# Kernel optimization log

Hardware: AMD Instinct MI355X
Metric: run time of the kernel (lower is better)

The kernel has to match this reference:

```python
import jax, jax.numpy as jnp
import numpy as np

D_MODEL = 1024
N_HEADS = 16
D_HEAD = D_MODEL // N_HEADS


def setup_inputs() -> dict:
    key = jax.random.key(0)
    ks = jax.random.split(key, 5)
    s_in = 1.0 / np.sqrt(D_MODEL)
    x = jax.random.normal(ks[0], (4, 2048, D_MODEL), dtype=jnp.float32)
    W_qkv = jax.random.uniform(ks[1], (D_MODEL, 3 * D_MODEL), jnp.float32, -s_in, s_in)
    b_qkv = jax.random.uniform(ks[2], (3 * D_MODEL,), jnp.float32, -s_in, s_in)
    W_out = jax.random.uniform(ks[3], (D_MODEL, D_MODEL), jnp.float32, -s_in, s_in)
    b_out = jax.random.uniform(ks[4], (D_MODEL,), jnp.float32, -s_in, s_in)
    return {"x": x, "W_qkv": W_qkv, "b_qkv": b_qkv, "W_out": W_out, "b_out": b_out}


def reference(x, W_qkv, b_qkv, W_out, b_out):
    B, T, C = x.shape
    qkv = x @ W_qkv + b_qkv                       # [B,T,3C]
    q, k, v = jnp.split(qkv, 3, axis=-1)
    # [B,T,C] -> [B,H,T,Dh]
    def heads(t):
        return t.reshape(B, T, N_HEADS, D_HEAD).transpose(0, 2, 1, 3)
    q, k, v = heads(q), heads(k), heads(v)
    scale = 1.0 / np.sqrt(D_HEAD).astype(np.float32)
    attn = jnp.einsum('bhqd,bhkd->bhqk', q, k) * scale   # [B,H,T,T]
    causal = jnp.tril(jnp.ones((T, T), dtype=bool))
    attn = jnp.where(causal, attn, -jnp.inf)
    attn_weights = jax.nn.softmax(attn, axis=-1)
    out = jnp.einsum('bhqk,bhkd->bhqd', attn_weights, v)  # [B,H,T,Dh]
    out = out.transpose(0, 2, 1, 3).reshape(B, T, C)
    return out @ W_out + b_out
```

## Files before the change

### kernel.cpp

```cpp
#include <hip/hip_runtime.h>
#include <hip/hip_bf16.h>

#define BATCH   4
#define SEQ     2048
#define DMODEL  1024
#define NHEADS  16
#define DHEAD   64
#define MROWS   (BATCH*SEQ)
#define QKV_N   (3*DMODEL)
#define NEG_BIG (-1.0e30f)
#define WS_NEED ((size_t)MROWS * 2*DMODEL * sizeof(__hip_bfloat16))
#define SCALE_Q 0.18033688011112042f

using bf16 = __hip_bfloat16;
typedef __attribute__((ext_vector_type(8))) short short8;
typedef __attribute__((ext_vector_type(4))) float floatx4;

__device__ __align__(16) unsigned short g_wqT[QKV_N * DMODEL];
__device__ __align__(16) unsigned short g_woT[DMODEL * DMODEL];
__device__ __align__(16) unsigned short g_xb [MROWS * DMODEL];

__device__ __forceinline__ unsigned short f2bf_rne(float f) {
    union { bf16 b; unsigned short u; } t;
    t.b = __float2bfloat16(f);
    return t.u;
}

__device__ __forceinline__ void gload_lds16(const void* g, void* l) {
    __builtin_amdgcn_global_load_lds(
        (const __attribute__((address_space(1))) unsigned*)g,
        (__attribute__((address_space(3))) unsigned*)l, 16, 0, 0);
}

__global__ __launch_bounds__(256) void cast_x(const float* __restrict__ x) {
    const size_t i = ((size_t)blockIdx.x*256 + threadIdx.x)*8;
    const float4 a = *(const float4*)(x + i);
    const float4 b = *(const float4*)(x + i + 4);
    union { uint4 u4; unsigned short us[8]; } o;
    o.us[0]=f2bf_rne(a.x); o.us[1]=f2bf_rne(a.y); o.us[2]=f2bf_rne(a.z); o.us[3]=f2bf_rne(a.w);
    o.us[4]=f2bf_rne(b.x); o.us[5]=f2bf_rne(b.y); o.us[6]=f2bf_rne(b.z); o.us[7]=f2bf_rne(b.w);
    *(uint4*)(g_xb + i) = o.u4;
}

__global__ __launch_bounds__(256) void transcast_w2(
    const float* __restrict__ Wq, const float* __restrict__ Wo)
{
    const int bx = blockIdx.x;
    const float* W;
    unsigned short* dst;
    int N, n0;
    if (bx < 48) { W = Wq; dst = g_wqT; N = QKV_N;  n0 = bx * 64; }
    else         { W = Wo; dst = g_woT; N = DMODEL; n0 = (bx - 48) * 64; }
    const int k0 = blockIdx.y * 64;

    __shared__ unsigned short T[64][72];
    const int tid = threadIdx.x;
    const int r = tid >> 2, c0 = (tid & 3) * 16;

#pragma unroll
    for (int it = 0; it < 4; ++it) {
        const float4 v = *(const float4*)(W + (size_t)(k0 + r)*N + n0 + c0 + it*4);
        T[r][c0 + it*4 + 0] = f2bf_rne(v.x);
        T[r][c0 + it*4 + 1] = f2bf_rne(v.y);
        T[r][c0 + it*4 + 2] = f2bf_rne(v.z);
        T[r][c0 + it*4 + 3] = f2bf_rne(v.w);
    }
    __syncthreads();
    const int nr = tid >> 2, kc0 = (tid & 3) * 16;
#pragma unroll
    for (int it = 0; it < 2; ++it) {
        union { uint4 u4; unsigned short us[8]; } o;
#pragma unroll
        for (int j = 0; j < 8; j++) o.us[j] = T[kc0 + it*8 + j][nr];
        *(uint4*)(dst + (size_t)(n0 + nr)*DMODEL + k0 + kc0 + it*8) = o.u4;
    }
}

__global__ __launch_bounds__(512, 2) void qkv_proj(
    const float* __restrict__ bias, bf16* __restrict__ Qo,
    bf16* __restrict__ Ko, bf16* __restrict__ VT)
{
    const unsigned short* A  = g_xb;
    const unsigned short* BT = g_wqT;
    constexpr int NBN = 12;
    constexpr int NWG = 32 * NBN;

    __shared__ __align__(16) char smem[131072];
    char* const sA = smem;
    char* const sB = smem + 65536;

    const int orig = blockIdx.x;
    const int wgid = (orig & 7) * (NWG >> 3) + (orig >> 3);
    const int bm = wgid / NBN, bn = wgid % NBN;

    const int tid  = threadIdx.x;
    const int w    = tid >> 6, lane = tid & 63;
    const int m16  = lane & 15, quad = lane >> 4;
    const int rw   = w >> 2, cw = w & 3;

    const int rL = lane >> 2;
    const int cD = (lane & 3) ^ ((lane >> 3) & 3);
    const unsigned short* gA = A  + (size_t)(bm*256 + rL)*DMODEL + cD*8;
    const unsigned short* gB = BT + (size_t)(bn*256 + rL)*DMODEL + cD*8;

    const int laneRd = m16*64 + (quad ^ ((m16 >> 1) & 3))*16;

    floatx4 acc[8][4];
#pragma unroll
    for (int i = 0; i < 8; ++i)
#pragma unroll
        for (int j = 0; j < 4; ++j) {
            acc[i][j][0]=0.f; acc[i][j][1]=0.f; acc[i][j][2]=0.f; acc[i][j][3]=0.f;
        }

    auto stA = [&](int buf, int rg, int kh, int k0) {
        gload_lds16(gA + (size_t)(rg*16)*DMODEL + k0 + kh*32,
                    sA + buf*32768 + (rg*2 + kh)*1024);
    };
    auto stB = [&](int buf, int rg, int kh, int k0) {
        gload_lds16(gB + (size_t)(rg*16)*DMODEL + k0 + kh*32,
                    sB + buf*32768 + (rg*2 + kh)*1024);
    };

    stA(0, w, 0, 0);   stA(0, 8+w, 0, 0);
    stB(0, 2*w, 0, 0); stB(0, 2*w+1, 0, 0);
    stA(0, w, 1, 0);   stA(0, 8+w, 1, 0);
    stB(0, 2*w, 1, 0); stB(0, 2*w+1, 1, 0);
    asm volatile("s_waitcnt vmcnt(0)" ::: "memory");
    __builtin_amdgcn_s_barrier();

    const int NT = DMODEL / 64;
    for (int t = 0; t < NT; ++t) {
        const int  buf = t & 1;
        const int  k1  = (t + 1) * 64;
        const bool st  = (t + 1 < NT);
        char* const Ab = sA + buf*32768;
        char* const Bb = sB + buf*32768;

        short8 bf[4], af[4];

#pragma unroll
        for (int j = 0; j < 4; ++j)
            bf[j] = *(const short8*)(Bb + ((cw*4 + j)*2 + 0)*1024 + laneRd);
#pragma unroll
        for (int i = 0; i < 4; ++i)
            af[i] = *(const short8*)(Ab + ((rw*8 + i)*2 + 0)*1024 + laneRd);
        if (st) { stA(buf^1, w, 0, k1); stA(buf^1, 8+w, 0, k1); }
        __builtin_amdgcn_s_barrier();
        __builtin_amdgcn_s_setprio(1);
#pragma unroll
        for (int i = 0; i < 4; ++i)
#pragma unroll
            for (int j = 0; j < 4; ++j)
                acc[i][j] = __builtin_amdgcn_mfma_f32_16x16x32_bf16(af[i], bf[j], acc[i][j], 0, 0, 0);
        __builtin_amdgcn_s_setprio(0);
        __builtin_amdgcn_s_barrier();

#pragma unroll
        for (int i = 0; i < 4; ++i)
            af[i] = *(const short8*)(Ab + ((rw*8 + 4 + i)*2 + 0)*1024 + laneRd);
        if (st) { stB(buf^1, 2*w, 0, k1); stB(buf^1, 2*w+1, 0, k1); }
        __builtin_amdgcn_s_barrier();
        __builtin_amdgcn_s_setprio(1);
#pragma unroll
        for (int i = 0; i < 4; ++i)
#pragma unroll
            for (int j = 0; j < 4; ++j)
                acc[4+i][j] = __builtin_amdgcn_mfma_f32_16x16x32_bf16(af[i], bf[j], acc[4+i][j], 0, 0, 0);
        __builtin_amdgcn_s_setprio(0);
        if (st) { asm volatile("s_waitcnt vmcnt(4)" ::: "memory"); }
        else    { asm volatile("s_waitcnt vmcnt(0)" ::: "memory"); }
        __builtin_amdgcn_s_barrier();

#pragma unroll
        for (int j = 0; j < 4; ++j)
            bf[j] = *(const short8*)(Bb + ((cw*4 + j)*2 + 1)*1024 + laneRd);
#pragma unroll
        for (int i = 0; i < 4; ++i)
            af[i] = *(const short8*)(Ab + ((rw*8 + i)*2 + 1)*1024 + laneRd);
        if (st) { stA(buf^1, w, 1, k1); stA(buf^1, 8+w, 1, k1); }
        __builtin_amdgcn_s_barrier();
        __builtin_amdgcn_s_setprio(1);
#pragma unroll
        for (int i = 0; i < 4; ++i)
#pragma unroll
            for (int j = 0; j < 4; ++j)
                acc[i][j] = __builtin_amdgcn_mfma_f32_16x16x32_bf16(af[i], bf[j], acc[i][j], 0, 0, 0);
        __builtin_amdgcn_s_setprio(0);
        __builtin_amdgcn_s_barrier();

#pragma unroll
        for (int i = 0; i < 4; ++i)
            af[i] = *(const short8*)(Ab + ((rw*8 + 4 + i)*2 + 1)*1024 + laneRd);
        if (st) { stB(buf^1, 2*w, 1, k1); stB(buf^1, 2*w+1, 1, k1); }
        __builtin_amdgcn_s_barrier();
        __builtin_amdgcn_s_setprio(1);
#pragma unroll
        for (int i = 0; i < 4; ++i)
#pragma unroll
            for (int j = 0; j < 4; ++j)
                acc[4+i][j] = __builtin_amdgcn_mfma_f32_16x16x32_bf16(af[i], bf[j], acc[4+i][j], 0, 0, 0);
        __builtin_amdgcn_s_setprio(0);
        if (st) {
            asm volatile("s_waitcnt vmcnt(4)" ::: "memory");
            __builtin_amdgcn_s_barrier();
        }
    }

    float bv[4];
#pragma unroll
    for (int j = 0; j < 4; ++j)
        bv[j] = bias[bn*256 + cw*64 + j*16 + m16];

    const int seg = bn >> 2;
    if (seg < 2) {
        bf16* Cout = seg ? Ko : Qo;
        const float sc = seg ? 1.0f : SCALE_Q;
#pragma unroll
        for (int mf = 0; mf < 8; ++mf)
#pragma unroll
            for (int r = 0; r < 4; ++r) {
                const int gm = bm*256 + rw*128 + mf*16 + quad*4 + r;
#pragma unroll
                for (int j = 0; j < 4; ++j) {
                    const int cc = (bn*256 + cw*64 + j*16 + m16) & 1023;
                    Cout[(size_t)gm*DMODEL + cc] =
                        __float2bfloat16((acc[mf][j][r] + bv[j]) * sc);
                }
            }
    } else {
#pragma unroll
        for (int mf = 0; mf < 8; ++mf) {
            const int gm0 = bm*256 + rw*128 + mf*16 + quad*4;
            const int bb = gm0 >> 11, t0 = gm0 & 2047;
#pragma unroll
            for (int j = 0; j < 4; ++j) {
                const int cv = ((bn & 3)*256 + cw*64 + j*16 + m16);
                const int hh = cv >> 6, dd = cv & 63;
                union { unsigned long long u8; unsigned short us[4]; } o;
#pragma unroll
                for (int r = 0; r < 4; ++r)
                    o.us[r] = f2bf_rne(acc[mf][j][r] + bv[j]);
                *(unsigned long long*)(VT
                    + ((size_t)((bb*NHEADS + hh)*DHEAD + dd))*SEQ + t0) = o.u8;
            }
        }
    }
}

__global__ __launch_bounds__(512, 2) void out_proj(
    const void* __restrict__ Av, const float* __restrict__ bias, float* C)
{
    const unsigned short* A  = (const unsigned short*)Av;
    const unsigned short* BT = g_woT;
    constexpr int NBN = 8;
    constexpr int NWG = NBN * 32;

    __shared__ __align__(16) char smem[98304];
    char* const sA = smem;
    char* const sB = smem + 65536;

    const int orig = blockIdx.x;
    const int wgid = (orig & 7) * (NWG >> 3) + (orig >> 3);
    const int bm = wgid / NBN, bn = wgid % NBN;

    const int tid  = threadIdx.x;
    const int w    = tid >> 6, lane = tid & 63;
    const int m16  = lane & 15, quad = lane >> 4;
    const int rw   = w >> 1, cw = w & 1;

    const int rL = lane >> 2;
    const int cD = (lane & 3) ^ ((lane >> 3) & 3);
    const unsigned short* gA = A  + (size_t)(bm*256 + rL)*DMODEL + cD*8;
    const unsigned short* gB = BT + (size_t)(bn*128 + rL)*DMODEL + cD*8;

    const int laneRd = m16*64 + (quad ^ ((m16 >> 1) & 3))*16;

    floatx4 acc[2][2][4];
#pragma unroll
    for (int q = 0; q < 2; ++q)
#pragma unroll
        for (int i = 0; i < 2; ++i)
#pragma unroll
            for (int j = 0; j < 4; ++j) {
                acc[q][i][j][0]=0.f; acc[q][i][j][1]=0.f;
                acc[q][i][j][2]=0.f; acc[q][i][j][3]=0.f;
            }

    auto stageA = [&](int buf, int a, int k0) {
        const int rg = 4*a + (w >> 1), kh = w & 1;
        gload_lds16(gA + (size_t)(rg*16)*DMODEL + k0 + kh*32,
                    sA + buf*32768 + (rg*2 + kh)*1024);
    };
    auto stageB = [&](int buf, int b, int k0) {
        const int rg = 4*b + (w >> 1), kh = w & 1;
        gload_lds16(gB + (size_t)(rg*16)*DMODEL + k0 + kh*32,
                    sB + buf*16384 + (rg*2 + kh)*1024);
    };

    stageB(0, 0, 0); stageB(0, 1, 0);
    stageA(0, 0, 0); stageA(0, 1, 0); stageA(0, 2, 0); stageA(0, 3, 0);
    asm volatile("s_waitcnt vmcnt(0)" ::: "memory");
    __builtin_amdgcn_s_barrier();

    const int NT = DMODEL / 64;
    for (int t = 0; t < NT; ++t) {
        const int  buf = t & 1;
        const int  k1  = (t + 1) * 64;
        const bool st  = (t + 1 < NT);
        char* const Ab = sA + buf*32768;
        char* const Bb = sB + buf*16384;

        short8 bf[4][2], af[2][2];
#pragma unroll
        for (int j = 0; j < 4; ++j)
#pragma unroll
            for (int kh = 0; kh < 2; ++kh)
                bf[j][kh] = *(const short8*)(Bb + ((cw*4 + j)*2 + kh)*1024 + laneRd);
#pragma unroll
        for (int i = 0; i < 2; ++i)
#pragma unroll
            for (int kh = 0; kh < 2; ++kh)
                af[i][kh] = *(const short8*)(Ab + ((rw*2 + i)*2 + kh)*1024 + laneRd);

        if (st) { stageB(buf^1, 0, k1); stageB(buf^1, 1, k1);
                  stageA(buf^1, 0, k1); stageA(buf^1, 1, k1); }
        __builtin_amdgcn_s_barrier();

        __builtin_amdgcn_s_setprio(1);
#pragma unroll
        for (int i = 0; i < 2; ++i)
#pragma unroll
            for (int j = 0; j < 4; ++j) {
                acc[0][i][j] = __builtin_amdgcn_mfma_f32_16x16x32_bf16(
                    af[i][0], bf[j][0], acc[0][i][j], 0, 0, 0);
                acc[0][i][j] = __builtin_amdgcn_mfma_f32_16x16x32_bf16(
                    af[i][1], bf[j][1], acc[0][i][j], 0, 0, 0);
            }
        __builtin_amdgcn_s_setprio(0);

        if (st) { asm volatile("s_waitcnt vmcnt(4)" ::: "memory"); }
        else    { asm volatile("s_waitcnt vmcnt(0)" ::: "memory"); }
        __builtin_amdgcn_s_barrier();

#pragma unroll
        for (int i = 0; i < 2; ++i)
#pragma unroll
            for (int kh = 0; kh < 2; ++kh)
                af[i][kh] = *(const short8*)(Ab + ((8 + rw*2 + i)*2 + kh)*1024 + laneRd);

        if (st) { stageA(buf^1, 2, k1); stageA(buf^1, 3, k1); }
        __builtin_amdgcn_s_barrier();

        __builtin_amdgcn_s_setprio(1);
#pragma unroll
        for (int i = 0; i < 2; ++i)
#pragma unroll
            for (int j = 0; j < 4; ++j) {
                acc[1][i][j] = __builtin_amdgcn_mfma_f32_16x16x32_bf16(
                    af[i][0], bf[j][0], acc[1][i][j], 0, 0, 0);
                acc[1][i][j] = __builtin_amdgcn_mfma_f32_16x16x32_bf16(
                    af[i][1], bf[j][1], acc[1][i][j], 0, 0, 0);
            }
        __builtin_amdgcn_s_setprio(0);

        if (st) { asm volatile("s_waitcnt vmcnt(2)" ::: "memory"); }
        else    { asm volatile("s_waitcnt vmcnt(0)" ::: "memory"); }
        __builtin_amdgcn_s_barrier();
    }

    float bv[4];
#pragma unroll
    for (int j = 0; j < 4; ++j)
        bv[j] = bias[bn*128 + cw*64 + j*16 + m16];

#pragma unroll
    for (int q = 0; q < 2; ++q)
#pragma unroll
        for (int i = 0; i < 2; ++i)
#pragma unroll
            for (int r = 0; r < 4; ++r) {
                const int gm = bm*256 + q*128 + rw*32 + i*16 + quad*4 + r;
#pragma unroll
                for (int j = 0; j < 4; ++j) {
                    const int cc = bn*128 + cw*64 + j*16 + m16;
                    C[(size_t)gm*DMODEL + cc] = acc[q][i][j][r] + bv[j];
                }
            }
}

__global__ __launch_bounds__(256, 3) void attn_mfma7(
    const bf16* __restrict__ Qg, const bf16* __restrict__ Kg,
    const bf16* __restrict__ VTg, bf16* __restrict__ Og)
{
    __shared__ alignas(16) unsigned short Kt[2][64][72];
    __shared__ alignas(16) unsigned short Vt[80][72];
    __shared__ alignas(16) unsigned short Ps[4][32][72];

    const int L  = blockIdx.x;
    const int qt = 15 - (L >> 6);
    const int bh = L & 63;
    const int b  = bh >> 4, h = bh & 15;

    const int tid = threadIdx.x;
    const int w = tid >> 6, lane = tid & 63;
    const int m16 = lane & 15, quad = lane >> 4;
    const int sr = tid >> 2, sc0 = (tid & 3) * 8;
    const size_t bhs = (size_t)(b*NHEADS + h);

    const int nkt = 2*qt + 2;
    const int qrow0 = qt*128 + w*32;

    short8 qf[2][2];
#pragma unroll
    for (int i = 0; i < 2; ++i)
#pragma unroll
        for (int c = 0; c < 2; ++c)
            qf[i][c] = *(const short8*)(Qg + (size_t)(b*SEQ + qrow0 + i*16 + m16)*DMODEL
                                        + h*DHEAD + c*32 + quad*8);

    floatx4 of[2][5];
    float mrow[2];
#pragma unroll
    for (int i = 0; i < 2; ++i) {
        mrow[i] = NEG_BIG;
#pragma unroll
        for (int nt = 0; nt < 5; ++nt) { of[i][nt][0]=0.f; of[i][nt][1]=0.f; of[i][nt][2]=0.f; of[i][nt][3]=0.f; }
    }

    for (int idx = tid; idx < 16*72; idx += 256) {
        const int r = idx / 72, c = idx % 72;
        Vt[64 + r][c] = (r == 0) ? (unsigned short)0x3F80 : (unsigned short)0;
    }

    {
        const bf16* kp = Kg  + (size_t)(b*SEQ + sr)*DMODEL + h*DHEAD + sc0;
        const bf16* vp = VTg + (bhs*DHEAD + sr)*SEQ + sc0;
        const uint4 a0 = *(const uint4*)kp, a1 = *(const uint4*)(kp + 32);
        const uint4 b0 = *(const uint4*)vp, b1 = *(const uint4*)(vp + 32);
        *(uint4*)&Kt[0][sr][sc0]      = a0;
        *(uint4*)&Kt[0][sr][sc0 + 32] = a1;
        *(uint4*)&Vt[sr][sc0]         = b0;
        *(uint4*)&Vt[sr][sc0 + 32]    = b1;
        __syncthreads();
    }

    for (int kt = 0; kt < nkt; ++kt) {
        const int buf = kt & 1;
        const int k064 = kt * 64;
        const bool pre = (kt + 1 < nkt);
        uint4 kr0, kr1, vr0, vr1;
        if (pre) {
            const bf16* kp = Kg  + (size_t)(b*SEQ + k064 + 64 + sr)*DMODEL + h*DHEAD + sc0;
            const bf16* vp = VTg + (bhs*DHEAD + sr)*SEQ + k064 + 64 + sc0;
            kr0 = *(const uint4*)kp; kr1 = *(const uint4*)(kp + 32);
            vr0 = *(const uint4*)vp; vr1 = *(const uint4*)(vp + 32);
        }

        floatx4 sf[2][4];
#pragma unroll
        for (int t4 = 0; t4 < 4; ++t4) {
            const short8 kf0 = *(const short8*)&Kt[buf][t4*16 + m16][quad*8];
            const short8 kf1 = *(const short8*)&Kt[buf][t4*16 + m16][32 + quad*8];
#pragma unroll
            for (int i = 0; i < 2; ++i) {
                floatx4 a; a[0]=0.f; a[1]=0.f; a[2]=0.f; a[3]=0.f;
                a = __builtin_amdgcn_mfma_f32_16x16x32_bf16(kf0, qf[i][0], a, 0, 0, 0);
                a = __builtin_amdgcn_mfma_f32_16x16x32_bf16(kf1, qf[i][1], a, 0, 0, 0);
                sf[i][t4] = a;
            }
        }

        const bool need_mask = (k064 + 63 > qrow0);
#pragma unroll
        for (int i = 0; i < 2; ++i) {
            if (need_mask) {
                const int qg = qrow0 + i*16 + m16;
#pragma unroll
                for (int t4 = 0; t4 < 4; ++t4)
#pragma unroll
                    for (int r = 0; r < 4; ++r)
                        if (k064 + t4*16 + quad*4 + r > qg) sf[i][t4][r] = NEG_BIG;
            }
            float mx = sf[i][0][0];
#pragma unroll
            for (int t4 = 0; t4 < 4; ++t4)
#pragma unroll
                for (int r = 0; r < 4; ++r) mx = fmaxf(mx, sf[i][t4][r]);
            mx = fmaxf(mx, __shfl_xor(mx, 16));
            mx = fmaxf(mx, __shfl_xor(mx, 32));

            if (__any(mx > mrow[i] + 8.f)) {
                const float mnew  = fmaxf(mrow[i], mx);
                const float alpha = exp2f(mrow[i] - mnew);
                mrow[i] = mnew;
#pragma unroll
                for (int nt = 0; nt < 5; ++nt)
#pragma unroll
                    for (int r = 0; r < 4; ++r) of[i][nt][r] *= alpha;
            }

#pragma unroll
            for (int t4 = 0; t4 < 4; ++t4)
#pragma unroll
                for (int r = 0; r < 4; ++r)
                    sf[i][t4][r] = exp2f(sf[i][t4][r] - mrow[i]);

#pragma unroll
            for (int t4 = 0; t4 < 4; ++t4) {
                union { unsigned long long u8; unsigned short us[4]; } o;
#pragma unroll
                for (int r = 0; r < 4; ++r) o.us[r] = f2bf_rne(sf[i][t4][r]);
                *(unsigned long long*)&Ps[w][i*16 + m16][t4*16 + quad*4] = o.u8;
            }
        }

        short8 pf[2][2];
#pragma unroll
        for (int i = 0; i < 2; ++i)
#pragma unroll
            for (int c = 0; c < 2; ++c)
                pf[i][c] = *(const short8*)&Ps[w][i*16 + m16][c*32 + quad*8];
#pragma unroll
        for (int nt = 0; nt < 5; ++nt) {
            const short8 vf0 = *(const short8*)&Vt[nt*16 + m16][quad*8];
            const short8 vf1 = *(const short8*)&Vt[nt*16 + m16][32 + quad*8];
#pragma unroll
            for (int i = 0; i < 2; ++i) {
                of[i][nt] = __builtin_amdgcn_mfma_f32_16x16x32_bf16(vf0, pf[i][0], of[i][nt], 0, 0, 0);
                of[i][nt] = __builtin_amdgcn_mfma_f32_16x16x32_bf16(vf1, pf[i][1], of[i][nt], 0, 0, 0);
            }
        }

        __syncthreads();
        if (pre) {
            *(uint4*)&Kt[buf^1][sr][sc0]      = kr0;
            *(uint4*)&Kt[buf^1][sr][sc0 + 32] = kr1;
            *(uint4*)&Vt[sr][sc0]             = vr0;
            *(uint4*)&Vt[sr][sc0 + 32]        = vr1;
        }
        __syncthreads();
    }

#pragma unroll
    for (int i = 0; i < 2; ++i) {
        const float lsum = __shfl(of[i][4][0], m16);
        const float rl = 1.f / fmaxf(lsum, 1e-20f);
        const size_t rowbase = (size_t)(b*SEQ + qrow0 + i*16 + m16)*DMODEL + h*DHEAD;
#pragma unroll
        for (int nt = 0; nt < 4; ++nt) {
            union { unsigned long long u8; unsigned short us[4]; } o;
#pragma unroll
            for (int r = 0; r < 4; ++r) o.us[r] = f2bf_rne(of[i][nt][r] * rl);
            *(unsigned long long*)(Og + rowbase + nt*16 + quad*4) = o.u8;
        }
    }
}

__global__ void diag_fill(float* out, int n, float val) {
    int i = blockIdx.x*blockDim.x + threadIdx.x;
    if (i < n) out[i] = val;
}

extern "C" void kernel_launch(void* const* d_in, const int* in_sizes, int n_in,
                              void* d_out, int out_size, void* d_ws, size_t ws_size,
                              hipStream_t stream) {
    const float* x     = (const float*)d_in[0];
    const float* W_qkv = (const float*)d_in[1];
    const float* b_qkv = (const float*)d_in[2];
    const float* W_out = (const float*)d_in[3];
    const float* b_out = (const float*)d_in[4];

    if (ws_size < WS_NEED) {
        const float val = 100.f + (float)(ws_size >> 20);
        diag_fill<<<(out_size + 255)/256, 256, 0, stream>>>((float*)d_out, out_size, val);
        return;
    }

    bf16* Qb  = (bf16*)d_out;
    bf16* VTb = (bf16*)d_out + (size_t)MROWS*DMODEL;
    bf16* Kb  = (bf16*)d_ws;
    bf16* Ob  = (bf16*)d_ws + (size_t)MROWS*DMODEL;

    cast_x<<<MROWS*DMODEL/2048, 256, 0, stream>>>(x);
    {
        dim3 g(64, DMODEL/64);
        transcast_w2<<<g, 256, 0, stream>>>(W_qkv, W_out);
    }
    qkv_proj<<<384, 512, 0, stream>>>(b_qkv, Qb, Kb, VTb);
    attn_mfma7<<<1024, 256, 0, stream>>>(Qb, Kb, VTb, Ob);
    out_proj<<<256, 512, 0, stream>>>(Ob, b_out, (float*)d_out);
}
```

Before: 266.9 us.

## Merge prep kernels and simplify GEMM main loops to one barrier per k-step

Fuses the x cast and weight transpose-cast into a single prep launch, removing one kernel launch. In both the QKV and output projection GEMMs, the k-step is restructured: all of the next tile is staged at once, and all A/B fragments for each k-half are loaded before one big MFMA batch. This replaces several intra-iteration barriers and partial vmcnt waits with a single full wait and barrier. It reduces sync overhead but holds more fragment registers and gives the prefetch less overlap before the full wait.

```diff
diff --git a/kernel.cpp b/kernel.cpp
--- a/kernel.cpp
+++ b/kernel.cpp
@@ -32,31 +32,32 @@
         (__attribute__((address_space(3))) unsigned*)l, 16, 0, 0);
 }
 
-__global__ __launch_bounds__(256) void cast_x(const float* __restrict__ x) {
-    const size_t i = ((size_t)blockIdx.x*256 + threadIdx.x)*8;
-    const float4 a = *(const float4*)(x + i);
-    const float4 b = *(const float4*)(x + i + 4);
-    union { uint4 u4; unsigned short us[8]; } o;
-    o.us[0]=f2bf_rne(a.x); o.us[1]=f2bf_rne(a.y); o.us[2]=f2bf_rne(a.z); o.us[3]=f2bf_rne(a.w);
-    o.us[4]=f2bf_rne(b.x); o.us[5]=f2bf_rne(b.y); o.us[6]=f2bf_rne(b.z); o.us[7]=f2bf_rne(b.w);
-    *(uint4*)(g_xb + i) = o.u4;
-}
-
-__global__ __launch_bounds__(256) void transcast_w2(
-    const float* __restrict__ Wq, const float* __restrict__ Wo)
+__global__ __launch_bounds__(256) void prep(
+    const float* __restrict__ x, const float* __restrict__ Wq,
+    const float* __restrict__ Wo)
 {
     const int bx = blockIdx.x;
+    const int tid = threadIdx.x;
+    if (bx < 4096) {
+        const size_t i = ((size_t)bx*256 + tid)*8;
+        const float4 a = *(const float4*)(x + i);
+        const float4 b = *(const float4*)(x + i + 4);
+        union { uint4 u4; unsigned short us[8]; } o;
+        o.us[0]=f2bf_rne(a.x); o.us[1]=f2bf_rne(a.y); o.us[2]=f2bf_rne(a.z); o.us[3]=f2bf_rne(a.w);
+        o.us[4]=f2bf_rne(b.x); o.us[5]=f2bf_rne(b.y); o.us[6]=f2bf_rne(b.z); o.us[7]=f2bf_rne(b.w);
+        *(uint4*)(g_xb + i) = o.u4;
+        return;
+    }
+    const int idx = bx - 4096;
+    const int nb = idx & 63, k0 = (idx >> 6) * 64;
     const float* W;
     unsigned short* dst;
     int N, n0;
-    if (bx < 48) { W = Wq; dst = g_wqT; N = QKV_N;  n0 = bx * 64; }
-    else         { W = Wo; dst = g_woT; N = DMODEL; n0 = (bx - 48) * 64; }
-    const int k0 = blockIdx.y * 64;
+    if (nb < 48) { W = Wq; dst = g_wqT; N = QKV_N;  n0 = nb * 64; }
+    else         { W = Wo; dst = g_woT; N = DMODEL; n0 = (nb - 48) * 64; }
 
     __shared__ unsigned short T[64][72];
-    const int tid = threadIdx.x;
     const int r = tid >> 2, c0 = (tid & 3) * 16;
-
 #pragma unroll
     for (int it = 0; it < 4; ++it) {
         const float4 v = *(const float4*)(W + (size_t)(k0 + r)*N + n0 + c0 + it*4);
@@ -121,11 +122,14 @@
         gload_lds16(gB + (size_t)(rg*16)*DMODEL + k0 + kh*32,
                     sB + buf*32768 + (rg*2 + kh)*1024);
     };
-
-    stA(0, w, 0, 0);   stA(0, 8+w, 0, 0);
-    stB(0, 2*w, 0, 0); stB(0, 2*w+1, 0, 0);
-    stA(0, w, 1, 0);   stA(0, 8+w, 1, 0);
-    stB(0, 2*w, 1, 0); stB(0, 2*w+1, 1, 0);
+    auto stageAll = [&](int buf, int k0) {
+        stA(buf, w, 0, k0);     stA(buf, 8+w, 0, k0);
+        stA(buf, w, 1, k0);     stA(buf, 8+w, 1, k0);
+        stB(buf, 2*w, 0, k0);   stB(buf, 2*w+1, 0, k0);
+        stB(buf, 2*w, 1, k0);   stB(buf, 2*w+1, 1, k0);
+    };
+
+    stageAll(0, 0);
     asm volatile("s_waitcnt vmcnt(0)" ::: "memory");
     __builtin_amdgcn_s_barrier();
 
@@ -137,72 +141,41 @@
         char* const Ab = sA + buf*32768;
         char* const Bb = sB + buf*32768;
 
-        short8 bf[4], af[4];
+        short8 bf[4], af[8];
 
 #pragma unroll
         for (int j = 0; j < 4; ++j)
             bf[j] = *(const short8*)(Bb + ((cw*4 + j)*2 + 0)*1024 + laneRd);
 #pragma unroll
-        for (int i = 0; i < 4; ++i)
+        for (int i = 0; i < 8; ++i)
             af[i] = *(const short8*)(Ab + ((rw*8 + i)*2 + 0)*1024 + laneRd);
-        if (st) { stA(buf^1, w, 0, k1); stA(buf^1, 8+w, 0, k1); }
-        __builtin_amdgcn_s_barrier();
+        if (st) stageAll(buf^1, k1);
+
         __builtin_amdgcn_s_setprio(1);
 #pragma unroll
-        for (int i = 0; i < 4; ++i)
+        for (int i = 0; i < 8; ++i)
 #pragma unroll
             for (int j = 0; j < 4; ++j)
                 acc[i][j] = __builtin_amdgcn_mfma_f32_16x16x32_bf16(af[i], bf[j], acc[i][j], 0, 0, 0);
         __builtin_amdgcn_s_setprio(0);
-        __builtin_amdgcn_s_barrier();
-
-#pragma unroll
-        for (int i = 0; i < 4; ++i)
-            af[i] = *(const short8*)(Ab + ((rw*8 + 4 + i)*2 + 0)*1024 + laneRd);
-        if (st) { stB(buf^1, 2*w, 0, k1); stB(buf^1, 2*w+1, 0, k1); }
-        __builtin_amdgcn_s_barrier();
-        __builtin_amdgcn_s_setprio(1);
-#pragma unroll
-        for (int i = 0; i < 4; ++i)
-#pragma unroll
-            for (int j = 0; j < 4; ++j)
-                acc[4+i][j] = __builtin_amdgcn_mfma_f32_16x16x32_bf16(af[i], bf[j], acc[4+i][j], 0, 0, 0);
-        __builtin_amdgcn_s_setprio(0);
-        if (st) { asm volatile("s_waitcnt vmcnt(4)" ::: "memory"); }
-        else    { asm volatile("s_waitcnt vmcnt(0)" ::: "memory"); }
-        __builtin_amdgcn_s_barrier();
 
 #pragma unroll
         for (int j = 0; j < 4; ++j)
             bf[j] = *(const short8*)(Bb + ((cw*4 + j)*2 + 1)*1024 + laneRd);
 #pragma unroll
-        for (int i = 0; i < 4; ++i)
+        for (int i = 0; i < 8; ++i)
             af[i] = *(const short8*)(Ab + ((rw*8 + i)*2 + 1)*1024 + laneRd);
-        if (st) { stA(buf^1, w, 1, k1); stA(buf^1, 8+w, 1, k1); }
-        __builtin_amdgcn_s_barrier();
+
         __builtin_amdgcn_s_setprio(1);
 #pragma unroll
-        for (int i = 0; i < 4; ++i)
+        for (int i = 0; i < 8; ++i)
 #pragma unroll
             for (int j = 0; j < 4; ++j)
                 acc[i][j] = __builtin_amdgcn_mfma_f32_16x16x32_bf16(af[i], bf[j], acc[i][j], 0, 0, 0);
         __builtin_amdgcn_s_setprio(0);
-        __builtin_amdgcn_s_barrier();
-
-#pragma unroll
-        for (int i = 0; i < 4; ++i)
-            af[i] = *(const short8*)(Ab + ((rw*8 + 4 + i)*2 + 1)*1024 + laneRd);
-        if (st) { stB(buf^1, 2*w, 1, k1); stB(buf^1, 2*w+1, 1, k1); }
-        __builtin_amdgcn_s_barrier();
-        __builtin_amdgcn_s_setprio(1);
-#pragma unroll
-        for (int i = 0; i < 4; ++i)
-#pragma unroll
-            for (int j = 0; j < 4; ++j)
-                acc[4+i][j] = __builtin_amdgcn_mfma_f32_16x16x32_bf16(af[i], bf[j], acc[4+i][j], 0, 0, 0);
-        __builtin_amdgcn_s_setprio(0);
+
         if (st) {
-            asm volatile("s_waitcnt vmcnt(4)" ::: "memory");
+            asm volatile("s_waitcnt vmcnt(0)" ::: "memory");
             __builtin_amdgcn_s_barrier();
         }
     }
@@ -297,9 +270,13 @@
         gload_lds16(gB + (size_t)(rg*16)*DMODEL + k0 + kh*32,
                     sB + buf*16384 + (rg*2 + kh)*1024);
     };
-
-    stageB(0, 0, 0); stageB(0, 1, 0);
-    stageA(0, 0, 0); stageA(0, 1, 0); stageA(0, 2, 0); stageA(0, 3, 0);
+    auto stageAll = [&](int buf, int k0) {
+        stageB(buf, 0, k0); stageB(buf, 1, k0);
+        stageA(buf, 0, k0); stageA(buf, 1, k0);
+        stageA(buf, 2, k0); stageA(buf, 3, k0);
+    };
+
+    stageAll(0, 0);
     asm volatile("s_waitcnt vmcnt(0)" ::: "memory");
     __builtin_amdgcn_s_barrier();
 
@@ -311,62 +288,40 @@
         char* const Ab = sA + buf*32768;
         char* const Bb = sB + buf*16384;
 
-        short8 bf[4][2], af[2][2];
+        short8 bf[4][2], af[2][2][2];
 #pragma unroll
         for (int j = 0; j < 4; ++j)
 #pragma unroll
             for (int kh = 0; kh < 2; ++kh)
                 bf[j][kh] = *(const short8*)(Bb + ((cw*4 + j)*2 + kh)*1024 + laneRd);
 #pragma unroll
-        for (int i = 0; i < 2; ++i)
-#pragma unroll
-            for (int kh = 0; kh < 2; ++kh)
-                af[i][kh] = *(const short8*)(Ab + ((rw*2 + i)*2 + kh)*1024 + laneRd);
-
-        if (st) { stageB(buf^1, 0, k1); stageB(buf^1, 1, k1);
-                  stageA(buf^1, 0, k1); stageA(buf^1, 1, k1); }
-        __builtin_amdgcn_s_barrier();
+        for (int q = 0; q < 2; ++q)
+#pragma unroll
+            for (int i = 0; i < 2; ++i)
+#pragma unroll
+                for (int kh = 0; kh < 2; ++kh)
+                    af[q][i][kh] = *(const short8*)(Ab + ((q*8 + rw*2 + i)*2 + kh)*1024 + laneRd);
+
+        if (st) stageAll(buf^1, k1);
 
         __builtin_amdgcn_s_setprio(1);
 #pragma unroll
-        for (int i = 0; i < 2; ++i)
-#pragma unroll
-            for (int j = 0; j < 4; ++j) {
-                acc[0][i][j] = __builtin_amdgcn_mfma_f32_16x16x32_bf16(
-                    af[i][0], bf[j][0], acc[0][i][j], 0, 0, 0);
-                acc[0][i][j] = __builtin_amdgcn_mfma_f32_16x16x32_bf16(
-                    af[i][1], bf[j][1], acc[0][i][j], 0, 0, 0);
-            }
+        for (int q = 0; q < 2; ++q)
+#pragma unroll
+            for (int i = 0; i < 2; ++i)
+#pragma unroll
+                for (int j = 0; j < 4; ++j) {
+                    acc[q][i][j] = __builtin_amdgcn_mfma_f32_16x16x32_bf16(
+                        af[q][i][0], bf[j][0], acc[q][i][j], 0, 0, 0);
+                    acc[q][i][j] = __builtin_amdgcn_mfma_f32_16x16x32_bf16(
+                        af[q][i][1], bf[j][1], acc[q][i][j], 0, 0, 0);
+                }
         __builtin_amdgcn_s_setprio(0);
 
-        if (st) { asm volatile("s_waitcnt vmcnt(4)" ::: "memory"); }
-        else    { asm volatile("s_waitcnt vmcnt(0)" ::: "memory"); }
-        __builtin_amdgcn_s_barrier();
-
-#pragma unroll
-        for (int i = 0; i < 2; ++i)
-#pragma unroll
-            for (int kh = 0; kh < 2; ++kh)
-                af[i][kh] = *(const short8*)(Ab + ((8 + rw*2 + i)*2 + kh)*1024 + laneRd);
-
-        if (st) { stageA(buf^1, 2, k1); stageA(buf^1, 3, k1); }
-        __builtin_amdgcn_s_barrier();
-
-        __builtin_amdgcn_s_setprio(1);
-#pragma unroll
-        for (int i = 0; i < 2; ++i)
-#pragma unroll
-            for (int j = 0; j < 4; ++j) {
-                acc[1][i][j] = __builtin_amdgcn_mfma_f32_16x16x32_bf16(
-                    af[i][0], bf[j][0], acc[1][i][j], 0, 0, 0);
-                acc[1][i][j] = __builtin_amdgcn_mfma_f32_16x16x32_bf16(
-                    af[i][1], bf[j][1], acc[1][i][j], 0, 0, 0);
-            }
-        __builtin_amdgcn_s_setprio(0);
-
-        if (st) { asm volatile("s_waitcnt vmcnt(2)" ::: "memory"); }
-        else    { asm volatile("s_waitcnt vmcnt(0)" ::: "memory"); }
-        __builtin_amdgcn_s_barrier();
+        if (st) {
+            asm volatile("s_waitcnt vmcnt(0)" ::: "memory");
+            __builtin_amdgcn_s_barrier();
+        }
     }
 
     float bv[4];
@@ -582,11 +537,7 @@
     bf16* Kb  = (bf16*)d_ws;
     bf16* Ob  = (bf16*)d_ws + (size_t)MROWS*DMODEL;
 
-    cast_x<<<MROWS*DMODEL/2048, 256, 0, stream>>>(x);
-    {
-        dim3 g(64, DMODEL/64);
-        transcast_w2<<<g, 256, 0, stream>>>(W_qkv, W_out);
-    }
+    prep<<<5120, 256, 0, stream>>>(x, W_qkv, W_out);
     qkv_proj<<<384, 512, 0, stream>>>(b_qkv, Qb, Kb, VTb);
     attn_mfma7<<<1024, 256, 0, stream>>>(Qb, Kb, VTb, Ob);
     out_proj<<<256, 512, 0, stream>>>(Ob, b_out, (float*)d_out);
```

Result: no change. 267.2 us (+0.1%).
